# Optimization experiments

Measured on AMD Instinct MI355X. Metric: run time of the kernel, lower is better.

Reference implementation:

```python
import jax, jax.numpy as jnp
import numpy as np

N = 100000   # nodes
E = 400000   # edges
G = 2048     # graphs in batch
H = 128      # hidden_channels
V = 100      # in_channels (element vocab)
L = 3        # hidden_layers (GAT)
LO = 2       # out_layers (dense)
SLOPE = 0.2  # GATConv negative_slope default


def setup_inputs() -> dict:
    key = jax.random.key(0)
    ks = jax.random.split(key, 14)
    s = 1.0 / np.sqrt(H)
    return {
        "x": jax.random.randint(ks[0], (N,), 0, V),
        "edge_index": jax.random.randint(ks[1], (2, E), 0, N),
        "edge_attr": jax.random.uniform(ks[2], (E, 1), dtype=jnp.float32),
        "batch": jnp.sort(jax.random.randint(ks[3], (N,), 0, G)),
        "emb": jax.random.normal(ks[4], (V, H), dtype=jnp.float32),
        "gat_W": jax.random.normal(ks[5], (L, H, H), dtype=jnp.float32) * s,
        "att_src": jax.random.normal(ks[6], (L, H), dtype=jnp.float32) * s,
        "att_dst": jax.random.normal(ks[7], (L, H), dtype=jnp.float32) * s,
        "edge_W": jax.random.normal(ks[8], (L, H), dtype=jnp.float32) * s,  # lin_edge: Linear(1, H, bias=False)
        "att_edge": jax.random.normal(ks[9], (L, H), dtype=jnp.float32) * s,
        "gat_b": jnp.zeros((L, H), dtype=jnp.float32),
        "lin_W": jax.random.normal(ks[10], (LO, H, H), dtype=jnp.float32) * s,
        "lin_b": jnp.zeros((LO, H), dtype=jnp.float32),
        "wp_W": jax.random.normal(ks[11], (H, 1), dtype=jnp.float32) * s,
        "wp_b": jnp.zeros((1,), dtype=jnp.float32),
    }


def _segment_softmax(logits, seg, num_segments):
    m = jax.ops.segment_max(logits, seg, num_segments=num_segments)
    e = jnp.exp(logits - m[seg])
    s = jax.ops.segment_sum(e, seg, num_segments=num_segments)
    return e / s[seg]


def reference(x, edge_index, edge_attr, batch, emb, gat_W, att_src, att_dst,
              edge_W, att_edge, gat_b, lin_W, lin_b, wp_W, wp_b):
    src, dst = edge_index[0], edge_index[1]
    # GATConv add_self_loops=True with fill_value='mean' for edge_attr
    loop = jnp.arange(N, dtype=src.dtype)
    src_sl = jnp.concatenate([src, loop])          # [E+N]
    dst_sl = jnp.concatenate([dst, loop])          # [E+N]
    ea_mean = jnp.mean(edge_attr, axis=0, keepdims=True)  # [1,1]
    ea_sl = jnp.concatenate([edge_attr, jnp.broadcast_to(ea_mean, (N, 1))], axis=0)  # [E+N,1]

    h = emb[x]  # [N,H]
    for l in range(L):
        xt = h @ gat_W[l]                 # shared lin_src/lin_dst, heads=1
        a_s = xt @ att_src[l]             # [N]
        a_d = xt @ att_dst[l]             # [N]
        a_e = (ea_sl * edge_W[l][None, :]) @ att_edge[l]  # lin_edge then att_edge: [E+N]
        alpha = jax.nn.leaky_relu(a_s[src_sl] + a_d[dst_sl] + a_e, negative_slope=SLOPE)
        alpha = _segment_softmax(alpha, dst_sl, N)
        out = jax.ops.segment_sum(xt[src_sl] * alpha[:, None], dst_sl, num_segments=N)
        out = out + gat_b[l]
        # F.normalize(h_x, 2, dim=1)
        nrm = jnp.linalg.norm(out, axis=1, keepdims=True)
        h = out / jnp.maximum(nrm, 1e-12)
    for i in range(LO):
        h = jax.nn.relu(h @ lin_W[i] + lin_b[i])
    m_x = jax.ops.segment_sum(h, batch, num_segments=G)  # scatter_sum readout [G,H]
    props = m_x @ wp_W + wp_b                            # [G,1]
    return jnp.squeeze(props, axis=1)                    # [G]
```

## Files before the change

### kernel.cpp

```cpp
#include <hip/hip_runtime.h>
#include <math.h>

#define N_NODES 100000
#define N_EDGES 400000
#define NG 2048
#define H 128
#define NV 100
#define NLAYERS 3
#define SLOPE 0.2f

#define SCAL_N 64

typedef __attribute__((ext_vector_type(8))) short bf16x8;
typedef __attribute__((ext_vector_type(4))) float f32x4;

__device__ __forceinline__ float wave_reduce_sum(float v){
  #pragma unroll
  for (int off = 32; off > 0; off >>= 1) v += __shfl_xor(v, off, 64);
  return v;
}
__device__ __forceinline__ unsigned short rne_bf16(float f){
  unsigned int u = __float_as_uint(f);
  u += 0x7FFF + ((u >> 16) & 1);
  return (unsigned short)(u >> 16);
}

#define PB_CONVW 320
#define PB_CONVE (PB_CONVW + 50)
#define PB_OUT   (PB_CONVE + 8)
#define PB_DOTS  (PB_OUT + 1)
#define PB_EASUM (PB_DOTS + 256)
#define PB_DEG   (PB_EASUM + 1954)
__global__ __launch_bounds__(256) void k_prep(
    const float* __restrict__ gat_W, const float* __restrict__ lin_W,
    unsigned short* __restrict__ Wf,
    const float* __restrict__ emb, unsigned short* __restrict__ embb,
    const float* __restrict__ ea, const float* __restrict__ ew,
    const float* __restrict__ ae, float* __restrict__ scal,
    const float* __restrict__ wp_b, float* __restrict__ out,
    const int* __restrict__ ei, int* __restrict__ deg,
    int* __restrict__ rank)
{
  int b = blockIdx.x, tid = threadIdx.x;
  if (b < PB_CONVW){
    int i = b*256 + tid;
    int m   = i >> 14;
    int r   = i & 16383;
    int k0i = r >> 12;
    int r3  = r & 4095;
    int ct  = r3 >> 9;
    int r4  = r3 & 511;
    int lane= r4 >> 3;
    int j   = r4 & 7;
    int q = lane >> 4, ln = lane & 15;
    int k = k0i*32 + q*8 + j;
    int n = ct*16 + ln;
    const float* src = (m < 3) ? (gat_W + m*16384) : (lin_W + (m-3)*16384);
    Wf[i] = rne_bf16(src[k*H + n]);
  } else if (b < PB_CONVE){
    int i = (b - PB_CONVW)*256 + tid;
    if (i < NV*H) embb[i] = rne_bf16(emb[i]);
  } else if (b < PB_OUT){
    int g = (b - PB_CONVE)*256 + tid;
    if (g < NG) out[g] = wp_b[0];
  } else if (b < PB_DOTS){
    int l = tid >> 6, ln = tid & 63;
    if (l < NLAYERS){
      float p = ew[l*H + ln]*ae[l*H + ln] + ew[l*H + ln + 64]*ae[l*H + ln + 64];
      p = wave_reduce_sum(p);
      if (ln == 0) atomicAdd(&scal[32 + l], p);
    }
  } else if (b < PB_EASUM){
    int i = (b - PB_DOTS)*256 + tid;
    int stride = 256*256;
    float v = 0.f;
    for (; i < N_EDGES; i += stride) v += ea[i];
    v = wave_reduce_sum(v);
    if ((tid & 63) == 0) atomicAdd(&scal[0], v);
  } else {
    int i = (b - PB_EASUM)*256 + tid;
    if (i < N_EDGES + N_NODES){
      int d = (i < N_EDGES) ? ei[N_EDGES + i] : (i - N_EDGES);
      rank[i] = atomicAdd(&deg[d], 1);
    }
  }
}

__global__ __launch_bounds__(256) void k_alloc(
    const int* __restrict__ deg, int* __restrict__ row_ptr, int* __restrict__ counter){
  __shared__ int wsum[4];
  __shared__ int base;
  int n = blockIdx.x * 256 + threadIdx.x;
  int d = (n < N_NODES) ? deg[n] : 0;
  int lane = threadIdx.x & 63, wid = threadIdx.x >> 6;
  int v = d;
  #pragma unroll
  for (int off = 1; off < 64; off <<= 1){
    int u = __shfl_up(v, off, 64);
    if (lane >= off) v += u;
  }
  if (lane == 63) wsum[wid] = v;
  __syncthreads();
  if (threadIdx.x == 0){
    int t0 = wsum[0], t1 = wsum[1], t2 = wsum[2], t3 = wsum[3];
    base = atomicAdd(counter, t0 + t1 + t2 + t3);
    wsum[0] = 0; wsum[1] = t0; wsum[2] = t0 + t1; wsum[3] = t0 + t1 + t2;
  }
  __syncthreads();
  if (n < N_NODES) row_ptr[n] = base + wsum[wid] + (v - d);
}

__global__ void k_scatter(const int* __restrict__ ei, const float* __restrict__ ea,
                          const float* __restrict__ scal, const int* __restrict__ row_ptr,
                          const int* __restrict__ rank, int* __restrict__ csr_src,
                          float* __restrict__ csr_ea){
  int i = blockIdx.x * blockDim.x + threadIdx.x;
  if (i >= N_EDGES + N_NODES) return;
  int s, d; float v;
  if (i < N_EDGES){ s = ei[i]; d = ei[N_EDGES + i]; v = ea[i]; }
  else            { s = d = i - N_EDGES; v = scal[0] * (1.0f / N_EDGES); }
  int pos = row_ptr[d] + rank[i];
  csr_src[pos] = s;
  csr_ea[pos]  = v;
}

__global__ __launch_bounds__(256, 4) void k_gemm(
    const unsigned short* __restrict__ Ab, const int* __restrict__ xmap,
    const unsigned short* __restrict__ Wf,
    unsigned short* __restrict__ Cb,
    const float* __restrict__ att1, const float* __restrict__ att2,
    float* __restrict__ a_s_out, float* __restrict__ a_d_out)
{
  __shared__ unsigned short lw[16384];
  int tid  = threadIdx.x;
  int w    = tid >> 6;
  int lane = tid & 63;
  int q    = lane >> 4;
  int ln   = lane & 15;
  int waveRow = blockIdx.x*128 + w*32;

  #pragma unroll
  for (int i = 0; i < 8; ++i){
    int base = (i*256 + w*64) * 8;
    __builtin_amdgcn_global_load_lds(
        (const __attribute__((address_space(1))) unsigned int*)(Wf + base + lane*8),
        (__attribute__((address_space(3))) unsigned int*)(lw + base),
        16, 0, 0);
  }

  bf16x8 af[2][4];
  #pragma unroll
  for (int m = 0; m < 2; ++m){
    int r = waveRow + m*16 + ln;
    if (r >= N_NODES) r = N_NODES - 1;
    if (xmap) r = xmap[r];
    const unsigned short* Ar = Ab + (size_t)r*H;
    #pragma unroll
    for (int k0i = 0; k0i < 4; ++k0i)
      af[m][k0i] = *(const bf16x8*)(Ar + k0i*32 + q*8);
  }
  __syncthreads();

  f32x4 acc[2][8];
  #pragma unroll
  for (int m = 0; m < 2; ++m)
    #pragma unroll
    for (int ct = 0; ct < 8; ++ct) acc[m][ct] = (f32x4){0.f,0.f,0.f,0.f};

  #pragma unroll
  for (int k0i = 0; k0i < 4; ++k0i){
    #pragma unroll
    for (int ct = 0; ct < 8; ++ct){
      bf16x8 bw = *(const bf16x8*)(lw + k0i*4096 + ct*512 + lane*8);
      #pragma unroll
      for (int m = 0; m < 2; ++m)
        acc[m][ct] = __builtin_amdgcn_mfma_f32_16x16x32_bf16(af[m][k0i], bw, acc[m][ct], 0,0,0);
    }
  }

  float as_l[8], ad_l[8];
  #pragma unroll
  for (int ct = 0; ct < 8; ++ct){ as_l[ct] = att1[ct*16+ln]; ad_l[ct] = att2[ct*16+ln]; }
  #pragma unroll
  for (int m = 0; m < 2; ++m){
    #pragma unroll
    for (int r = 0; r < 4; ++r){
      int grow = waveRow + m*16 + q*4 + r;
      bool ok = grow < N_NODES;
      float ps = 0.f, pd = 0.f;
      #pragma unroll
      for (int ct = 0; ct < 8; ++ct){
        float v = acc[m][ct][r];
        if (ok) Cb[(size_t)grow*H + ct*16 + ln] = rne_bf16(v);
        ps += v * as_l[ct]; pd += v * ad_l[ct];
      }
      #pragma unroll
      for (int mk = 8; mk > 0; mk >>= 1){
        ps += __shfl_xor(ps, mk, 64);
        pd += __shfl_xor(pd, mk, 64);
      }
      if (ok && ln == 0){ a_s_out[grow] = ps; a_d_out[grow] = pd; }
    }
  }
}

__global__ __launch_bounds__(256, 4) void k_dense(
    const unsigned short* __restrict__ Ab,
    const unsigned short* __restrict__ Wf,
    const float* __restrict__ b1, const float* __restrict__ b2,
    const float* __restrict__ wp, const int* __restrict__ batch,
    float* __restrict__ out)
{
  __shared__ unsigned short lw[16384];
  int tid  = threadIdx.x;
  int w    = tid >> 6;
  int lane = tid & 63;
  int q    = lane >> 4;
  int ln   = lane & 15;
  int waveRow = blockIdx.x*128 + w*32;

  #pragma unroll
  for (int i = 0; i < 8; ++i){
    int base = (i*256 + w*64) * 8;
    __builtin_amdgcn_global_load_lds(
        (const __attribute__((address_space(1))) unsigned int*)(Wf + base + lane*8),
        (__attribute__((address_space(3))) unsigned int*)(lw + base),
        16, 0, 0);
  }
  bf16x8 af[2][4];
  #pragma unroll
  for (int m = 0; m < 2; ++m){
    int r = waveRow + m*16 + ln;
    if (r >= N_NODES) r = N_NODES - 1;
    const unsigned short* Ar = Ab + (size_t)r*H;
    #pragma unroll
    for (int k0i = 0; k0i < 4; ++k0i)
      af[m][k0i] = *(const bf16x8*)(Ar + k0i*32 + q*8);
  }
  __syncthreads();

  f32x4 acc[2][8];
  #pragma unroll
  for (int m = 0; m < 2; ++m)
    #pragma unroll
    for (int ct = 0; ct < 8; ++ct) acc[m][ct] = (f32x4){0.f,0.f,0.f,0.f};
  #pragma unroll
  for (int k0i = 0; k0i < 4; ++k0i){
    #pragma unroll
    for (int ct = 0; ct < 8; ++ct){
      bf16x8 bw = *(const bf16x8*)(lw + k0i*4096 + ct*512 + lane*8);
      #pragma unroll
      for (int m = 0; m < 2; ++m)
        acc[m][ct] = __builtin_amdgcn_mfma_f32_16x16x32_bf16(af[m][k0i], bw, acc[m][ct], 0,0,0);
    }
  }
  __syncthreads();

  unsigned short* lh = lw + (w << 12);
  float b1_l[8];
  #pragma unroll
  for (int ct = 0; ct < 8; ++ct) b1_l[ct] = b1[ct*16+ln];
  #pragma unroll
  for (int m = 0; m < 2; ++m){
    #pragma unroll
    for (int r = 0; r < 4; ++r){
      int lr = m*16 + q*4 + r;
      int sw = (lr & 7) << 3;
      #pragma unroll
      for (int ct = 0; ct < 8; ++ct){
        int col = ct*16 + ln;
        lh[lr*128 + (col ^ sw)] = rne_bf16(fmaxf(acc[m][ct][r] + b1_l[ct], 0.f));
      }
    }
  }
  __syncthreads();

  bf16x8 af2[2][4];
  #pragma unroll
  for (int m = 0; m < 2; ++m){
    int lr = m*16 + ln;
    int sw = (lr & 7) << 3;
    #pragma unroll
    for (int k0i = 0; k0i < 4; ++k0i)
      af2[m][k0i] = *(const bf16x8*)(lh + lr*128 + ((k0i*32 + q*8) ^ sw));
  }
  __syncthreads();

  #pragma unroll
  for (int i = 0; i < 8; ++i){
    int base = (i*256 + w*64) * 8;
    __builtin_amdgcn_global_load_lds(
        (const __attribute__((address_space(1))) unsigned int*)(Wf + 16384 + base + lane*8),
        (__attribute__((address_space(3))) unsigned int*)(lw + base),
        16, 0, 0);
  }
  __syncthreads();

  #pragma unroll
  for (int m = 0; m < 2; ++m)
    #pragma unroll
    for (int ct = 0; ct < 8; ++ct) acc[m][ct] = (f32x4){0.f,0.f,0.f,0.f};
  #pragma unroll
  for (int k0i = 0; k0i < 4; ++k0i){
    #pragma unroll
    for (int ct = 0; ct < 8; ++ct){
      bf16x8 bw = *(const bf16x8*)(lw + k0i*4096 + ct*512 + lane*8);
      #pragma unroll
      for (int m = 0; m < 2; ++m)
        acc[m][ct] = __builtin_amdgcn_mfma_f32_16x16x32_bf16(af2[m][k0i], bw, acc[m][ct], 0,0,0);
    }
  }

  float b2_l[8], wp_l[8];
  #pragma unroll
  for (int ct = 0; ct < 8; ++ct){ b2_l[ct] = b2[ct*16+ln]; wp_l[ct] = wp[ct*16+ln]; }
  #pragma unroll
  for (int m = 0; m < 2; ++m){
    #pragma unroll
    for (int r = 0; r < 4; ++r){
      int grow = waveRow + m*16 + q*4 + r;
      bool ok = grow < N_NODES;
      float ps = 0.f;
      #pragma unroll
      for (int ct = 0; ct < 8; ++ct)
        ps += fmaxf(acc[m][ct][r] + b2_l[ct], 0.f) * wp_l[ct];
      #pragma unroll
      for (int mk = 8; mk > 0; mk >>= 1) ps += __shfl_xor(ps, mk, 64);
      if (ok && ln == 0) atomicAdd(&out[batch[grow]], ps);
    }
  }
}

__global__ __launch_bounds__(256, 4) void k_aggregate(
    const uint2* __restrict__ xtb2, const float* __restrict__ a_s,
    const float* __restrict__ a_d, const int* __restrict__ csr_src,
    const float* __restrict__ csr_ea, const int* __restrict__ row_ptr,
    const int* __restrict__ deg, const float* __restrict__ scal, int l,
    const float* __restrict__ bias, uint2* __restrict__ hb2)
{
  __shared__ int2 lsw[4][2][32];
  int wid  = threadIdx.x >> 6;
  int lane = threadIdx.x & 63;
  int h    = lane >> 5;
  int c    = lane & 31;
  int n    = blockIdx.x*8 + wid*2 + h;
  if (n >= N_NODES) return;
  int beg = row_ptr[n];
  int d   = deg[n];
  float adn = a_d[n];
  float dl  = scal[32 + l];
  int maxd = max(d, __shfl_xor(d, 32, 64));

  float4 acc = make_float4(0.f,0.f,0.f,0.f);
  float ss = 0.f;
  for (int base = 0; base < maxd; base += 32){
    int s = 0; float wgt = 0.f;
    int j = base + c;
    if (j < d){
      int e = beg + j;
      s = csr_src[e];
      float lg = a_s[s] + adn + dl*csr_ea[e];
      lg = (lg > 0.f) ? lg : SLOPE*lg;
      wgt = __expf(lg);
    }
    int2 pk; pk.x = s; pk.y = __float_as_int(wgt);
    lsw[wid][h][c] = pk;

    int cnt8 = (min(32, maxd - base) + 7) & ~7;
    for (int j0 = 0; j0 < cnt8; j0 += 8){
      int2 sw[8];
      #pragma unroll
      for (int u = 0; u < 8; ++u) sw[u] = lsw[wid][h][j0 + u];
      uint2 xv[8];
      #pragma unroll
      for (int u = 0; u < 8; ++u)
        xv[u] = xtb2[(size_t)sw[u].x*(H/4) + c];
      #pragma unroll
      for (int u = 0; u < 8; ++u){
        float wgt8 = __int_as_float(sw[u].y);
        float x0 = __uint_as_float(xv[u].x << 16);
        float x1 = __uint_as_float(xv[u].x & 0xFFFF0000u);
        float x2 = __uint_as_float(xv[u].y << 16);
        float x3 = __uint_as_float(xv[u].y & 0xFFFF0000u);
        ss    += wgt8;
        acc.x += wgt8 * x0;
        acc.y += wgt8 * x1;
        acc.z += wgt8 * x2;
        acc.w += wgt8 * x3;
      }
    }
  }

  float4 bv = *(const float4*)(bias + c*4);
  float inv = 1.0f / ss;
  acc.x = acc.x*inv + bv.x;
  acc.y = acc.y*inv + bv.y;
  acc.z = acc.z*inv + bv.z;
  acc.w = acc.w*inv + bv.w;
  float sq = acc.x*acc.x + acc.y*acc.y + acc.z*acc.z + acc.w*acc.w;
  #pragma unroll
  for (int off = 16; off > 0; off >>= 1) sq += __shfl_xor(sq, off, 64);
  float rn = 1.0f / fmaxf(sqrtf(sq), 1e-12f);
  uint2 o;
  o.x = ((unsigned int)rne_bf16(acc.y*rn) << 16) | rne_bf16(acc.x*rn);
  o.y = ((unsigned int)rne_bf16(acc.w*rn) << 16) | rne_bf16(acc.z*rn);
  hb2[(size_t)n*(H/4) + c] = o;
}

extern "C" void kernel_launch(void* const* d_in, const int* in_sizes, int n_in,
                              void* d_out, int out_size, void* d_ws, size_t ws_size,
                              hipStream_t stream) {
  const int*   x          = (const int*)  d_in[0];
  const int*   edge_index = (const int*)  d_in[1];
  const float* edge_attr  = (const float*)d_in[2];
  const int*   batch      = (const int*)  d_in[3];
  const float* emb        = (const float*)d_in[4];
  const float* gat_W      = (const float*)d_in[5];
  const float* att_src    = (const float*)d_in[6];
  const float* att_dst    = (const float*)d_in[7];
  const float* edge_W     = (const float*)d_in[8];
  const float* att_edge   = (const float*)d_in[9];
  const float* gat_b      = (const float*)d_in[10];
  const float* lin_W      = (const float*)d_in[11];
  const float* lin_b      = (const float*)d_in[12];
  const float* wp_W       = (const float*)d_in[13];
  const float* wp_b       = (const float*)d_in[14];
  float* out = (float*)d_out;

  unsigned short* hb  = (unsigned short*)d_ws;
  unsigned short* xtb = hb + (size_t)N_NODES*H;
  unsigned short* Wt  = xtb + (size_t)N_NODES*H;
  unsigned short* embb= Wt + 5*16384;
  float* a_s    = (float*)(embb + NV*H);
  float* a_d    = a_s + N_NODES;
  float* csr_ea = a_d + N_NODES;
  float* scal   = csr_ea + (N_EDGES + N_NODES);
  int*   deg    = (int*)(scal + SCAL_N);
  int*   rank   = deg + N_NODES;
  int*   row_ptr= rank + (N_EDGES + N_NODES);
  int*   csr_src= row_ptr + N_NODES;

  hipMemsetAsync(scal, 0, (size_t)(SCAL_N + N_NODES) * sizeof(float), stream);

  k_prep<<<PB_DEG, 256, 0, stream>>>(
      gat_W, lin_W, Wt, emb, embb, edge_attr, edge_W, att_edge, scal,
      wp_b, out, edge_index, deg, rank);
  k_alloc<<<(N_NODES + 255)/256, 256, 0, stream>>>(deg, row_ptr, (int*)&scal[48]);
  k_scatter<<<(N_EDGES + N_NODES + 255)/256, 256, 0, stream>>>(
      edge_index, edge_attr, scal, row_ptr, rank, csr_src, csr_ea);

  const int gemm_grid = (N_NODES + 127) / 128;
  for (int l = 0; l < NLAYERS; ++l){
    k_gemm<<<gemm_grid, 256, 0, stream>>>(
        (l == 0) ? embb : hb, (l == 0) ? x : nullptr,
        Wt + (size_t)l*16384, xtb,
        att_src + l*H, att_dst + l*H, a_s, a_d);
    k_aggregate<<<(N_NODES + 7)/8, 256, 0, stream>>>(
        (const uint2*)xtb, a_s, a_d, csr_src, csr_ea, row_ptr, deg,
        scal, l, gat_b + l*H, (uint2*)hb);
  }
  k_dense<<<gemm_grid, 256, 0, stream>>>(
      hb, Wt + (size_t)3*16384, lin_b, lin_b + H, wp_W, batch, out);
}
```

Baseline: 305.4 us.

## Fuse GAT aggregation with next layer's GEMM and dense head via LDS tiles

Each layer's neighbour aggregation now runs inside the kernel that performs the following linear transform. A wave aggregates 32 nodes into a swizzled LDS slab, and that slab feeds the MFMA GEMM directly. The final aggregation is fused into the dense head the same way. This removes the hidden-state round trip through global memory and three kernel launches, and ping-pong buffers for xt and attention scores prevent read/write races across blocks. In exchange, aggregation parallelism drops from 8 nodes per block to 32 per wave processed serially, so latency hiding for the irregular gathers may get worse.

After: 312.4 us. 2.3% more time.

```diff
diff --git a/kernel.cpp b/kernel.cpp
--- a/kernel.cpp
+++ b/kernel.cpp
@@ -204,20 +204,202 @@
   }
 }
 
-__global__ __launch_bounds__(256, 4) void k_dense(
-    const unsigned short* __restrict__ Ab,
+__device__ __forceinline__ void aggregate_tile(
+    const uint2* __restrict__ xtb2, const float* __restrict__ a_s,
+    const float* __restrict__ a_d, const int* __restrict__ csr_src,
+    const float* __restrict__ csr_ea, const int* __restrict__ row_ptr,
+    const int* __restrict__ deg, float dl, const float* __restrict__ bias,
+    unsigned short* slab, int2 (*lsw)[32], int waveRow, int lane)
+{
+  int h = lane >> 5;
+  int c = lane & 31;
+  float4 bv = *(const float4*)(bias + c*4);
+  #pragma unroll 1
+  for (int it = 0; it < 16; ++it){
+    int lr = it*2 + h;
+    int n  = waveRow + lr;
+    bool valid = (n < N_NODES);
+    int beg = 0, dd = 0; float adn = 0.f;
+    if (valid){ beg = row_ptr[n]; dd = deg[n]; adn = a_d[n]; }
+    int maxd = max(dd, __shfl_xor(dd, 32, 64));
+    float4 acc = make_float4(0.f,0.f,0.f,0.f);
+    float ss = 0.f;
+    for (int base = 0; base < maxd; base += 32){
+      int s = 0; float wgt = 0.f;
+      int j = base + c;
+      if (j < dd){
+        int e = beg + j;
+        s = csr_src[e];
+        float lg = a_s[s] + adn + dl*csr_ea[e];
+        lg = (lg > 0.f) ? lg : SLOPE*lg;
+        wgt = __expf(lg);
+      }
+      int2 pk; pk.x = s; pk.y = __float_as_int(wgt);
+      lsw[h][c] = pk;
+
+      int cnt8 = (min(32, maxd - base) + 7) & ~7;
+      for (int j0 = 0; j0 < cnt8; j0 += 8){
+        int2 sw8[8];
+        #pragma unroll
+        for (int u = 0; u < 8; ++u) sw8[u] = lsw[h][j0 + u];
+        uint2 xv[8];
+        #pragma unroll
+        for (int u = 0; u < 8; ++u)
+          xv[u] = xtb2[(size_t)sw8[u].x*(H/4) + c];
+        #pragma unroll
+        for (int u = 0; u < 8; ++u){
+          float wg = __int_as_float(sw8[u].y);
+          float x0 = __uint_as_float(xv[u].x << 16);
+          float x1 = __uint_as_float(xv[u].x & 0xFFFF0000u);
+          float x2 = __uint_as_float(xv[u].y << 16);
+          float x3 = __uint_as_float(xv[u].y & 0xFFFF0000u);
+          ss    += wg;
+          acc.x += wg * x0;
+          acc.y += wg * x1;
+          acc.z += wg * x2;
+          acc.w += wg * x3;
+        }
+      }
+    }
+    float inv = 1.0f / ss;
+    float ax = acc.x*inv + bv.x;
+    float ay = acc.y*inv + bv.y;
+    float az = acc.z*inv + bv.z;
+    float aw = acc.w*inv + bv.w;
+    float sq = ax*ax + ay*ay + az*az + aw*aw;
+    #pragma unroll
+    for (int off = 16; off > 0; off >>= 1) sq += __shfl_xor(sq, off, 64);
+    float rn = 1.0f / fmaxf(sqrtf(sq), 1e-12f);
+    uint2 o;
+    o.x = ((unsigned int)rne_bf16(ay*rn) << 16) | rne_bf16(ax*rn);
+    o.y = ((unsigned int)rne_bf16(aw*rn) << 16) | rne_bf16(az*rn);
+    if (!valid){ o.x = 0u; o.y = 0u; }
+    int swz = (lr & 7) << 3;
+    *(uint2*)(slab + lr*128 + ((c*4) ^ swz)) = o;
+  }
+}
+
+__global__ __launch_bounds__(256, 4) void k_fused_gat(
+    const uint2* __restrict__ xtb_in, const float* __restrict__ a_s_in,
+    const float* __restrict__ a_d_in, const int* __restrict__ csr_src,
+    const float* __restrict__ csr_ea, const int* __restrict__ row_ptr,
+    const int* __restrict__ deg, const float* __restrict__ scal, int l,
+    const float* __restrict__ agg_bias,
+    const unsigned short* __restrict__ Wf,
+    unsigned short* __restrict__ xtb_out,
+    const float* __restrict__ att1, const float* __restrict__ att2,
+    float* __restrict__ a_s_out, float* __restrict__ a_d_out)
+{
+  __shared__ unsigned short lw[16384];
+  __shared__ int2 lsw[4][2][32];
+  int tid  = threadIdx.x;
+  int w    = tid >> 6;
+  int lane = tid & 63;
+  int q    = lane >> 4;
+  int ln   = lane & 15;
+  int waveRow = blockIdx.x*128 + w*32;
+  unsigned short* slab = lw + (w << 12);
+
+  aggregate_tile(xtb_in, a_s_in, a_d_in, csr_src, csr_ea, row_ptr, deg,
+                 scal[32 + l], agg_bias, slab, lsw[w], waveRow, lane);
+
+  bf16x8 af[2][4];
+  #pragma unroll
+  for (int m = 0; m < 2; ++m){
+    int lr = m*16 + ln;
+    int swz = (lr & 7) << 3;
+    #pragma unroll
+    for (int k0i = 0; k0i < 4; ++k0i)
+      af[m][k0i] = *(const bf16x8*)(slab + lr*128 + ((k0i*32 + q*8) ^ swz));
+  }
+  __syncthreads();
+
+  #pragma unroll
+  for (int i = 0; i < 8; ++i){
+    int base = (i*256 + w*64) * 8;
+    __builtin_amdgcn_global_load_lds(
+        (const __attribute__((address_space(1))) unsigned int*)(Wf + base + lane*8),
+        (__attribute__((address_space(3))) unsigned int*)(lw + base),
+        16, 0, 0);
+  }
+  __syncthreads();
+
+  f32x4 acc[2][8];
+  #pragma unroll
+  for (int m = 0; m < 2; ++m)
+    #pragma unroll
+    for (int ct = 0; ct < 8; ++ct) acc[m][ct] = (f32x4){0.f,0.f,0.f,0.f};
+  #pragma unroll
+  for (int k0i = 0; k0i < 4; ++k0i){
+    #pragma unroll
+    for (int ct = 0; ct < 8; ++ct){
+      bf16x8 bw = *(const bf16x8*)(lw + k0i*4096 + ct*512 + lane*8);
+      #pragma unroll
+      for (int m = 0; m < 2; ++m)
+        acc[m][ct] = __builtin_amdgcn_mfma_f32_16x16x32_bf16(af[m][k0i], bw, acc[m][ct], 0,0,0);
+    }
+  }
+
+  float as_l[8], ad_l[8];
+  #pragma unroll
+  for (int ct = 0; ct < 8; ++ct){ as_l[ct] = att1[ct*16+ln]; ad_l[ct] = att2[ct*16+ln]; }
+  #pragma unroll
+  for (int m = 0; m < 2; ++m){
+    #pragma unroll
+    for (int r = 0; r < 4; ++r){
+      int grow = waveRow + m*16 + q*4 + r;
+      bool ok = grow < N_NODES;
+      float ps = 0.f, pd = 0.f;
+      #pragma unroll
+      for (int ct = 0; ct < 8; ++ct){
+        float v = acc[m][ct][r];
+        if (ok) xtb_out[(size_t)grow*H + ct*16 + ln] = rne_bf16(v);
+        ps += v * as_l[ct]; pd += v * ad_l[ct];
+      }
+      #pragma unroll
+      for (int mk = 8; mk > 0; mk >>= 1){
+        ps += __shfl_xor(ps, mk, 64);
+        pd += __shfl_xor(pd, mk, 64);
+      }
+      if (ok && ln == 0){ a_s_out[grow] = ps; a_d_out[grow] = pd; }
+    }
+  }
+}
+
+__global__ __launch_bounds__(256, 4) void k_fused_dense(
+    const uint2* __restrict__ xtb_in, const float* __restrict__ a_s_in,
+    const float* __restrict__ a_d_in, const int* __restrict__ csr_src,
+    const float* __restrict__ csr_ea, const int* __restrict__ row_ptr,
+    const int* __restrict__ deg, const float* __restrict__ scal, int l,
+    const float* __restrict__ agg_bias,
     const unsigned short* __restrict__ Wf,
     const float* __restrict__ b1, const float* __restrict__ b2,
     const float* __restrict__ wp, const int* __restrict__ batch,
     float* __restrict__ out)
 {
   __shared__ unsigned short lw[16384];
+  __shared__ int2 lsw[4][2][32];
   int tid  = threadIdx.x;
   int w    = tid >> 6;
   int lane = tid & 63;
   int q    = lane >> 4;
   int ln   = lane & 15;
   int waveRow = blockIdx.x*128 + w*32;
+  unsigned short* slab = lw + (w << 12);
+
+  aggregate_tile(xtb_in, a_s_in, a_d_in, csr_src, csr_ea, row_ptr, deg,
+                 scal[32 + l], agg_bias, slab, lsw[w], waveRow, lane);
+
+  bf16x8 af[2][4];
+  #pragma unroll
+  for (int m = 0; m < 2; ++m){
+    int lr = m*16 + ln;
+    int swz = (lr & 7) << 3;
+    #pragma unroll
+    for (int k0i = 0; k0i < 4; ++k0i)
+      af[m][k0i] = *(const bf16x8*)(slab + lr*128 + ((k0i*32 + q*8) ^ swz));
+  }
+  __syncthreads();
 
   #pragma unroll
   for (int i = 0; i < 8; ++i){
@@ -227,16 +409,6 @@
         (__attribute__((address_space(3))) unsigned int*)(lw + base),
         16, 0, 0);
   }
-  bf16x8 af[2][4];
-  #pragma unroll
-  for (int m = 0; m < 2; ++m){
-    int r = waveRow + m*16 + ln;
-    if (r >= N_NODES) r = N_NODES - 1;
-    const unsigned short* Ar = Ab + (size_t)r*H;
-    #pragma unroll
-    for (int k0i = 0; k0i < 4; ++k0i)
-      af[m][k0i] = *(const bf16x8*)(Ar + k0i*32 + q*8);
-  }
   __syncthreads();
 
   f32x4 acc[2][8];
@@ -256,7 +428,6 @@
   }
   __syncthreads();
 
-  unsigned short* lh = lw + (w << 12);
   float b1_l[8];
   #pragma unroll
   for (int ct = 0; ct < 8; ++ct) b1_l[ct] = b1[ct*16+ln];
@@ -265,24 +436,22 @@
     #pragma unroll
     for (int r = 0; r < 4; ++r){
       int lr = m*16 + q*4 + r;
-      int sw = (lr & 7) << 3;
+      int swz = (lr & 7) << 3;
       #pragma unroll
       for (int ct = 0; ct < 8; ++ct){
         int col = ct*16 + ln;
-        lh[lr*128 + (col ^ sw)] = rne_bf16(fmaxf(acc[m][ct][r] + b1_l[ct], 0.f));
-      }
-    }
-  }
-  __syncthreads();
-
+        slab[lr*128 + (col ^ swz)] = rne_bf16(fmaxf(acc[m][ct][r] + b1_l[ct], 0.f));
+      }
+    }
+  }
   bf16x8 af2[2][4];
   #pragma unroll
   for (int m = 0; m < 2; ++m){
     int lr = m*16 + ln;
-    int sw = (lr & 7) << 3;
+    int swz = (lr & 7) << 3;
     #pragma unroll
     for (int k0i = 0; k0i < 4; ++k0i)
-      af2[m][k0i] = *(const bf16x8*)(lh + lr*128 + ((k0i*32 + q*8) ^ sw));
+      af2[m][k0i] = *(const bf16x8*)(slab + lr*128 + ((k0i*32 + q*8) ^ swz));
   }
   __syncthreads();
 
@@ -329,82 +498,6 @@
       if (ok && ln == 0) atomicAdd(&out[batch[grow]], ps);
     }
   }
-}
-
-__global__ __launch_bounds__(256, 4) void k_aggregate(
-    const uint2* __restrict__ xtb2, const float* __restrict__ a_s,
-    const float* __restrict__ a_d, const int* __restrict__ csr_src,
-    const float* __restrict__ csr_ea, const int* __restrict__ row_ptr,
-    const int* __restrict__ deg, const float* __restrict__ scal, int l,
-    const float* __restrict__ bias, uint2* __restrict__ hb2)
-{
-  __shared__ int2 lsw[4][2][32];
-  int wid  = threadIdx.x >> 6;
-  int lane = threadIdx.x & 63;
-  int h    = lane >> 5;
-  int c    = lane & 31;
-  int n    = blockIdx.x*8 + wid*2 + h;
-  if (n >= N_NODES) return;
-  int beg = row_ptr[n];
-  int d   = deg[n];
-  float adn = a_d[n];
-  float dl  = scal[32 + l];
-  int maxd = max(d, __shfl_xor(d, 32, 64));
-
-  float4 acc = make_float4(0.f,0.f,0.f,0.f);
-  float ss = 0.f;
-  for (int base = 0; base < maxd; base += 32){
-    int s = 0; float wgt = 0.f;
-    int j = base + c;
-    if (j < d){
-      int e = beg + j;
-      s = csr_src[e];
-      float lg = a_s[s] + adn + dl*csr_ea[e];
-      lg = (lg > 0.f) ? lg : SLOPE*lg;
-      wgt = __expf(lg);
-    }
-    int2 pk; pk.x = s; pk.y = __float_as_int(wgt);
-    lsw[wid][h][c] = pk;
-
-    int cnt8 = (min(32, maxd - base) + 7) & ~7;
-    for (int j0 = 0; j0 < cnt8; j0 += 8){
-      int2 sw[8];
-      #pragma unroll
-      for (int u = 0; u < 8; ++u) sw[u] = lsw[wid][h][j0 + u];
-      uint2 xv[8];
-      #pragma unroll
-      for (int u = 0; u < 8; ++u)
-        xv[u] = xtb2[(size_t)sw[u].x*(H/4) + c];
-      #pragma unroll
-      for (int u = 0; u < 8; ++u){
-        float wgt8 = __int_as_float(sw[u].y);
-        float x0 = __uint_as_float(xv[u].x << 16);
-        float x1 = __uint_as_float(xv[u].x & 0xFFFF0000u);
-        float x2 = __uint_as_float(xv[u].y << 16);
-        float x3 = __uint_as_float(xv[u].y & 0xFFFF0000u);
-        ss    += wgt8;
-        acc.x += wgt8 * x0;
-        acc.y += wgt8 * x1;
-        acc.z += wgt8 * x2;
-        acc.w += wgt8 * x3;
-      }
-    }
-  }
-
-  float4 bv = *(const float4*)(bias + c*4);
-  float inv = 1.0f / ss;
-  acc.x = acc.x*inv + bv.x;
-  acc.y = acc.y*inv + bv.y;
-  acc.z = acc.z*inv + bv.z;
-  acc.w = acc.w*inv + bv.w;
-  float sq = acc.x*acc.x + acc.y*acc.y + acc.z*acc.z + acc.w*acc.w;
-  #pragma unroll
-  for (int off = 16; off > 0; off >>= 1) sq += __shfl_xor(sq, off, 64);
-  float rn = 1.0f / fmaxf(sqrtf(sq), 1e-12f);
-  uint2 o;
-  o.x = ((unsigned int)rne_bf16(acc.y*rn) << 16) | rne_bf16(acc.x*rn);
-  o.y = ((unsigned int)rne_bf16(acc.w*rn) << 16) | rne_bf16(acc.z*rn);
-  hb2[(size_t)n*(H/4) + c] = o;
 }
 
 extern "C" void kernel_launch(void* const* d_in, const int* in_sizes, int n_in,
@@ -427,13 +520,15 @@
   const float* wp_b       = (const float*)d_in[14];
   float* out = (float*)d_out;
 
-  unsigned short* hb  = (unsigned short*)d_ws;
-  unsigned short* xtb = hb + (size_t)N_NODES*H;
-  unsigned short* Wt  = xtb + (size_t)N_NODES*H;
-  unsigned short* embb= Wt + 5*16384;
-  float* a_s    = (float*)(embb + NV*H);
-  float* a_d    = a_s + N_NODES;
-  float* csr_ea = a_d + N_NODES;
+  unsigned short* xtbA = (unsigned short*)d_ws;
+  unsigned short* xtbB = xtbA + (size_t)N_NODES*H;
+  unsigned short* Wt   = xtbB + (size_t)N_NODES*H;
+  unsigned short* embb = Wt + 5*16384;
+  float* a_sA   = (float*)(embb + NV*H);
+  float* a_dA   = a_sA + N_NODES;
+  float* a_sB   = a_dA + N_NODES;
+  float* a_dB   = a_sB + N_NODES;
+  float* csr_ea = a_dB + N_NODES;
   float* scal   = csr_ea + (N_EDGES + N_NODES);
   int*   deg    = (int*)(scal + SCAL_N);
   int*   rank   = deg + N_NODES;
@@ -450,15 +545,18 @@
       edge_index, edge_attr, scal, row_ptr, rank, csr_src, csr_ea);
 
   const int gemm_grid = (N_NODES + 127) / 128;
-  for (int l = 0; l < NLAYERS; ++l){
-    k_gemm<<<gemm_grid, 256, 0, stream>>>(
-        (l == 0) ? embb : hb, (l == 0) ? x : nullptr,
-        Wt + (size_t)l*16384, xtb,
-        att_src + l*H, att_dst + l*H, a_s, a_d);
-    k_aggregate<<<(N_NODES + 7)/8, 256, 0, stream>>>(
-        (const uint2*)xtb, a_s, a_d, csr_src, csr_ea, row_ptr, deg,
-        scal, l, gat_b + l*H, (uint2*)hb);
-  }
-  k_dense<<<gemm_grid, 256, 0, stream>>>(
-      hb, Wt + (size_t)3*16384, lin_b, lin_b + H, wp_W, batch, out);
-}
+  k_gemm<<<gemm_grid, 256, 0, stream>>>(
+      embb, x, Wt, xtbA, att_src, att_dst, a_sA, a_dA);
+  k_fused_gat<<<gemm_grid, 256, 0, stream>>>(
+      (const uint2*)xtbA, a_sA, a_dA, csr_src, csr_ea, row_ptr, deg,
+      scal, 0, gat_b, Wt + (size_t)1*16384, xtbB,
+      att_src + H, att_dst + H, a_sB, a_dB);
+  k_fused_gat<<<gemm_grid, 256, 0, stream>>>(
+      (const uint2*)xtbB, a_sB, a_dB, csr_src, csr_ea, row_ptr, deg,
+      scal, 1, gat_b + H, Wt + (size_t)2*16384, xtbA,
+      att_src + 2*H, att_dst + 2*H, a_sA, a_dA);
+  k_fused_dense<<<gemm_grid, 256, 0, stream>>>(
+      (const uint2*)xtbA, a_sA, a_dA, csr_src, csr_ea, row_ptr, deg,
+      scal, 2, gat_b + 2*H, Wt + (size_t)3*16384,
+      lin_b, lin_b + H, wp_W, batch, out);
+}
```
